# Performance work log

Measured on AMD Instinct MI355X. Metric: run time of the kernel, lower is better.

Reference implementation:

```python
import jax, jax.numpy as jnp
import numpy as np

TEMP = 1.0
NUM_HEADS = 4


def tropical_linear(x, W, b, temperature=TEMP):
    # x: (..., in), W: (out, in), b: (out,)
    # y_i = T * logsumexp_j((W_ij + x_j)/T) + b_i  (soft tropical max-plus)
    z = W + x[..., None, :]                      # (..., out, in) broadcast tensor
    y = temperature * jax.nn.logsumexp(z / temperature, axis=-1)
    return y + b


def setup_inputs() -> dict:
    key = jax.random.key(0)
    ks = jax.random.split(key, 5)
    B, S, E = 32, 64, 256  # seq_len == head_dim (= E / num_heads) required by original code
    x = jax.random.normal(ks[0], (B, S, E), dtype=jnp.float32)
    mk = lambda k: 0.1 * jax.random.normal(k, (E, E), dtype=jnp.float32)
    zb = jnp.zeros((E,), dtype=jnp.float32)
    return {
        "x": x,
        "Wq": mk(ks[1]), "bq": zb,
        "Wk": mk(ks[2]), "bk": zb,
        "Wv": mk(ks[3]), "bv": zb,
        "Wo": mk(ks[4]), "bo": zb,
    }


def reference(x, Wq, bq, Wk, bk, Wv, bv, Wo, bo):
    B, S, E = x.shape
    H = NUM_HEADS
    D = E // H  # == S by construction (required by original matmul)

    q = tropical_linear(x, Wq, bq)  # (B,S,E)
    k = tropical_linear(x, Wk, bk)
    v = tropical_linear(x, Wv, bv)

    # (B,S,E) -> (B,H,S,D)
    split = lambda t: t.reshape(B, S, H, D).transpose(0, 2, 1, 3)
    q, k, v = split(q), split(k), split(v)

    # Original: (q.unsqueeze(-1) + k.unsqueeze(-2).transpose(-1,-2)).sum(-1)
    # Both operands are (B,H,S,D,1) -> scores == q + k elementwise, shape (B,H,S,D).
    scores = q + k
    attn = jax.nn.softmax(scores / TEMP, axis=-1)  # (B,H,S,D)

    # matmul (B,H,S,D) @ (B,H,S,D) valid since D == S
    out = jnp.einsum('bhsd,bhde->bhse', attn, v)   # (B,H,S,D)
    out = out.transpose(0, 2, 1, 3).reshape(B, S, E)
    return tropical_linear(out, Wo, bo)
```

## Files before the change

kernel.cpp:

```cpp
#include <hip/hip_runtime.h>

constexpr int ED = 256;
constexpr int SD = 64;
constexpr int BD = 32;
constexpr int NROWS = BD * SD;
constexpr int RB = 4;

__device__ inline unsigned short f2bf(float f) {
  unsigned u = __float_as_uint(f);
  return (unsigned short)((u + 0x7fffu + ((u >> 16) & 1u)) >> 16);
}
__device__ inline float bf2f(unsigned short b) {
  return __uint_as_float(((unsigned)b) << 16);
}

__global__ __launch_bounds__(256) void expT_pack_kernel(
    const float* __restrict__ Wq, const float* __restrict__ Wk,
    const float* __restrict__ Wv, const float* __restrict__ Wo,
    unsigned int* __restrict__ EqkT, unsigned short* __restrict__ EvT,
    unsigned short* __restrict__ EoT)
{
  __shared__ float ta[32][33], tb[32][33];
  int tx = threadIdx.x & 31, ty = threadIdx.x >> 5;
  int i0 = blockIdx.y * 32, j0 = blockIdx.x * 32;
  const float* A = blockIdx.z ? Wv : Wq;
  const float* Bm = blockIdx.z ? Wo : Wk;
#pragma unroll
  for (int r = 0; r < 4; r++) {
    ta[ty + 8 * r][tx] = __expf(A [(i0 + ty + 8 * r) * ED + j0 + tx]);
    tb[ty + 8 * r][tx] = __expf(Bm[(i0 + ty + 8 * r) * ED + j0 + tx]);
  }
  __syncthreads();
  if (blockIdx.z == 0) {
#pragma unroll
    for (int r = 0; r < 4; r++)
      EqkT[(j0 + ty + 8 * r) * ED + i0 + tx] =
          ((unsigned)f2bf(tb[tx][ty + 8 * r]) << 16) | f2bf(ta[tx][ty + 8 * r]);
  } else {
#pragma unroll
    for (int r = 0; r < 4; r++) {
      EvT[(j0 + ty + 8 * r) * ED + i0 + tx] = f2bf(ta[tx][ty + 8 * r]);
      EoT[(j0 + ty + 8 * r) * ED + i0 + tx] = f2bf(tb[tx][ty + 8 * r]);
    }
  }
}

__global__ __launch_bounds__(1024, 8) void qkv_kernel(
    const float* __restrict__ x,
    const unsigned int* __restrict__ EqkT, const unsigned short* __restrict__ EvT,
    const float* __restrict__ bq, const float* __restrict__ bk,
    const float* __restrict__ bv,
    float* __restrict__ attn, float* __restrict__ vout)
{
  int tid = threadIdx.x;
  int wv = tid >> 6, lane = tid & 63;
  int g = tid >> 8, t = tid & 255;
  int row0 = blockIdx.x * RB;

  __shared__ float eT[ED][RB];
  __shared__ float part[3][RB][ED][4];
  __shared__ float red[RB][4];

  {
    int pr = wv & 3, ps = wv >> 2;
    float xv = x[(size_t)(row0 + pr) * ED + ps * 64 + lane];
    float m = xv;
#pragma unroll
    for (int off = 32; off > 0; off >>= 1) m = fmaxf(m, __shfl_xor(m, off));
    if (lane == 0) red[pr][ps] = m;
    __syncthreads();
    float M = fmaxf(fmaxf(red[pr][0], red[pr][1]), fmaxf(red[pr][2], red[pr][3]));
    eT[ps * 64 + lane][pr] = __expf(xv - M);
  }
  __syncthreads();

  float aq[RB] = {0, 0, 0, 0}, ak[RB] = {0, 0, 0, 0}, av_[RB] = {0, 0, 0, 0};
  const unsigned int*  pqk = EqkT + (size_t)(64 * g) * ED + t;
  const unsigned short* pv = EvT + (size_t)(64 * g) * ED + t;
#pragma unroll 4
  for (int j = 0; j < 64; ++j) {
    float4 e4 = *(const float4*)eT[64 * g + j];
    unsigned int wqk = pqk[j * ED];
    float wvv = bf2f(pv[j * ED]);
    float wq = __uint_as_float(wqk << 16);
    float wk = __uint_as_float(wqk & 0xffff0000u);
    aq[0] = fmaf(wq, e4.x, aq[0]);  ak[0] = fmaf(wk, e4.x, ak[0]);  av_[0] = fmaf(wvv, e4.x, av_[0]);
    aq[1] = fmaf(wq, e4.y, aq[1]);  ak[1] = fmaf(wk, e4.y, ak[1]);  av_[1] = fmaf(wvv, e4.y, av_[1]);
    aq[2] = fmaf(wq, e4.z, aq[2]);  ak[2] = fmaf(wk, e4.z, ak[2]);  av_[2] = fmaf(wvv, e4.z, av_[2]);
    aq[3] = fmaf(wq, e4.w, aq[3]);  ak[3] = fmaf(wk, e4.w, ak[3]);  av_[3] = fmaf(wvv, e4.w, av_[3]);
  }

#pragma unroll
  for (int r = 0; r < RB; r++) {
    part[0][r][t][g] = aq[r];
    part[1][r][t][g] = ak[r];
    part[2][r][t][g] = av_[r];
  }
  __syncthreads();

  float4 q4 = *(const float4*)part[0][g][t];
  float4 k4 = *(const float4*)part[1][g][t];
  float4 v4 = *(const float4*)part[2][g][t];
  float fq = (q4.x + q4.y) + (q4.z + q4.w);
  float fk = (k4.x + k4.y) + (k4.z + k4.w);
  float fv = (v4.x + v4.y) + (v4.z + v4.w);
  float Mr = fmaxf(fmaxf(red[g][0], red[g][1]), fmaxf(red[g][2], red[g][3]));
  float qv = Mr + __logf(fq) + bq[t];
  float kv = Mr + __logf(fk) + bk[t];
  float vv = Mr + __logf(fv) + bv[t];
  vout[(size_t)(row0 + g) * ED + t] = vv;
  float s = qv + kv;
  float sm = s;
#pragma unroll
  for (int off = 32; off > 0; off >>= 1) sm = fmaxf(sm, __shfl_xor(sm, off));
  float ex = __expf(s - sm);
  float den = ex;
#pragma unroll
  for (int off = 32; off > 0; off >>= 1) den += __shfl_xor(den, off);
  attn[(size_t)(row0 + g) * ED + t] = ex / den;
}

__global__ __launch_bounds__(1024, 8) void avo_kernel(
    const float* __restrict__ attn, const float* __restrict__ vbuf,
    const unsigned short* __restrict__ EoT, const float* __restrict__ bo,
    float* __restrict__ y)
{
  int tid = threadIdx.x;
  int wv = tid >> 6, lane = tid & 63;
  int g = tid >> 8, t = tid & 255;
  int b = blockIdx.x >> 4;
  int row0 = b * SD + (blockIdx.x & 15) * RB;

  __shared__ float att[RB][ED];
  __shared__ float part[RB][ED][4];
  __shared__ float eoT[ED][RB];
  __shared__ float red[RB][4];

  att[g][t] = attn[(size_t)(row0 + g) * ED + t];
  float vr[16];
#pragma unroll
  for (int d = 0; d < 16; ++d)
    vr[d] = vbuf[(size_t)(b * SD + 16 * g + d) * ED + t];
  __syncthreads();

  int h64 = (t >> 6) << 6;
  float acc[RB];
#pragma unroll
  for (int r = 0; r < RB; ++r) {
    const float4* ap = (const float4*)&att[r][h64 + 16 * g];
    float a = 0.f;
#pragma unroll
    for (int d4 = 0; d4 < 4; ++d4) {
      float4 a4 = ap[d4];
      a = fmaf(a4.x, vr[4 * d4 + 0], a);
      a = fmaf(a4.y, vr[4 * d4 + 1], a);
      a = fmaf(a4.z, vr[4 * d4 + 2], a);
      a = fmaf(a4.w, vr[4 * d4 + 3], a);
    }
    acc[r] = a;
  }
#pragma unroll
  for (int r = 0; r < RB; ++r) part[r][t][g] = acc[r];
  __syncthreads();

  float4 p4 = *(const float4*)part[g][t];
  float orow = (p4.x + p4.y) + (p4.z + p4.w);
  float m = orow;
#pragma unroll
  for (int off = 32; off > 0; off >>= 1) m = fmaxf(m, __shfl_xor(m, off));
  if (lane == 0) red[g][wv & 3] = m;
  __syncthreads();
  float M = fmaxf(fmaxf(red[g][0], red[g][1]), fmaxf(red[g][2], red[g][3]));
  eoT[t][g] = __expf(orow - M);
  __syncthreads();

  float acc2[RB] = {0, 0, 0, 0};
  const unsigned short* po = EoT + (size_t)(64 * g) * ED + t;
#pragma unroll 4
  for (int j = 0; j < 64; ++j) {
    float4 e4 = *(const float4*)eoT[64 * g + j];
    float wo = bf2f(po[j * ED]);
    acc2[0] = fmaf(wo, e4.x, acc2[0]);
    acc2[1] = fmaf(wo, e4.y, acc2[1]);
    acc2[2] = fmaf(wo, e4.z, acc2[2]);
    acc2[3] = fmaf(wo, e4.w, acc2[3]);
  }
  __syncthreads();
#pragma unroll
  for (int r = 0; r < RB; ++r) part[r][t][g] = acc2[r];
  __syncthreads();

  float4 f4 = *(const float4*)part[g][t];
  float f = (f4.x + f4.y) + (f4.z + f4.w);
  y[(size_t)(row0 + g) * ED + t] = M + __logf(f) + bo[t];
}

extern "C" void kernel_launch(void* const* d_in, const int* in_sizes, int n_in,
                              void* d_out, int out_size, void* d_ws, size_t ws_size,
                              hipStream_t stream) {
  const float* x  = (const float*)d_in[0];
  const float* Wq = (const float*)d_in[1];
  const float* bq = (const float*)d_in[2];
  const float* Wk = (const float*)d_in[3];
  const float* bk = (const float*)d_in[4];
  const float* Wv = (const float*)d_in[5];
  const float* bv = (const float*)d_in[6];
  const float* Wo = (const float*)d_in[7];
  const float* bo = (const float*)d_in[8];
  float* y = (float*)d_out;

  char* ws = (char*)d_ws;
  unsigned int*   EqkT = (unsigned int*)(ws);
  unsigned short* EvT  = (unsigned short*)(ws + 262144);
  unsigned short* EoT  = (unsigned short*)(ws + 393216);
  float* attn = (float*)(ws + 524288);
  float* vbuf = (float*)(ws + 524288 + (size_t)NROWS * ED * 4);

  expT_pack_kernel<<<dim3(8, 8, 2), 256, 0, stream>>>(Wq, Wk, Wv, Wo,
                                                      EqkT, EvT, EoT);
  qkv_kernel<<<NROWS / RB, 1024, 0, stream>>>(x, EqkT, EvT, bq, bk, bv,
                                              attn, vbuf);
  avo_kernel<<<NROWS / RB, 1024, 0, stream>>>(attn, vbuf, EoT, bo, y);
}
```

Measured before the change: 98.72 us.

## Compute QKV tropical projections with bf16 MFMA on swizzled exp-weights

```diff
diff --git a/kernel.cpp b/kernel.cpp
--- a/kernel.cpp
+++ b/kernel.cpp
@@ -6,6 +6,9 @@
 constexpr int NROWS = BD * SD;
 constexpr int RB = 4;
 
+typedef short short8 __attribute__((ext_vector_type(8)));
+typedef float floatx4 __attribute__((ext_vector_type(4)));
+
 __device__ inline unsigned short f2bf(float f) {
   unsigned u = __float_as_uint(f);
   return (unsigned short)((u + 0x7fffu + ((u >> 16) & 1u)) >> 16);
@@ -14,110 +17,130 @@
   return __uint_as_float(((unsigned)b) << 16);
 }
 
-__global__ __launch_bounds__(256) void expT_pack_kernel(
+__global__ __launch_bounds__(256) void expT_swz_kernel(
     const float* __restrict__ Wq, const float* __restrict__ Wk,
-    const float* __restrict__ Wv, const float* __restrict__ Wo,
-    unsigned int* __restrict__ EqkT, unsigned short* __restrict__ EvT,
-    unsigned short* __restrict__ EoT)
-{
-  __shared__ float ta[32][33], tb[32][33];
+    const float* __restrict__ Wv,
+    unsigned short* __restrict__ EqS, unsigned short* __restrict__ EkS,
+    unsigned short* __restrict__ EvS)
+{
+  int z = blockIdx.y;
+  const float* W = (z == 0) ? Wq : (z == 1) ? Wk : Wv;
+  unsigned short* out = (z == 0) ? EqS : (z == 1) ? EkS : EvS;
+  int t = threadIdx.x;
+  int n = blockIdx.x * 8 + (t >> 5), kl = t & 31;
+#pragma unroll
+  for (int kk = 0; kk < 8; ++kk) {
+    float v = __expf(W[n * ED + 32 * kk + kl]);
+    out[(kk * 256 + n) * 32 + kl] = f2bf(v);
+  }
+}
+
+__global__ __launch_bounds__(256) void expT_o_kernel(
+    const float* __restrict__ Wo, unsigned short* __restrict__ EoT)
+{
+  __shared__ float ta[32][33];
   int tx = threadIdx.x & 31, ty = threadIdx.x >> 5;
   int i0 = blockIdx.y * 32, j0 = blockIdx.x * 32;
-  const float* A = blockIdx.z ? Wv : Wq;
-  const float* Bm = blockIdx.z ? Wo : Wk;
-#pragma unroll
-  for (int r = 0; r < 4; r++) {
-    ta[ty + 8 * r][tx] = __expf(A [(i0 + ty + 8 * r) * ED + j0 + tx]);
-    tb[ty + 8 * r][tx] = __expf(Bm[(i0 + ty + 8 * r) * ED + j0 + tx]);
-  }
-  __syncthreads();
-  if (blockIdx.z == 0) {
-#pragma unroll
-    for (int r = 0; r < 4; r++)
-      EqkT[(j0 + ty + 8 * r) * ED + i0 + tx] =
-          ((unsigned)f2bf(tb[tx][ty + 8 * r]) << 16) | f2bf(ta[tx][ty + 8 * r]);
-  } else {
-#pragma unroll
-    for (int r = 0; r < 4; r++) {
-      EvT[(j0 + ty + 8 * r) * ED + i0 + tx] = f2bf(ta[tx][ty + 8 * r]);
-      EoT[(j0 + ty + 8 * r) * ED + i0 + tx] = f2bf(tb[tx][ty + 8 * r]);
-    }
-  }
-}
-
-__global__ __launch_bounds__(1024, 8) void qkv_kernel(
+#pragma unroll
+  for (int r = 0; r < 4; r++)
+    ta[ty + 8 * r][tx] = __expf(Wo[(i0 + ty + 8 * r) * ED + j0 + tx]);
+  __syncthreads();
+#pragma unroll
+  for (int r = 0; r < 4; r++)
+    EoT[(j0 + ty + 8 * r) * ED + i0 + tx] = f2bf(ta[tx][ty + 8 * r]);
+}
+
+__global__ __launch_bounds__(256, 4) void qkv_mfma_kernel(
     const float* __restrict__ x,
-    const unsigned int* __restrict__ EqkT, const unsigned short* __restrict__ EvT,
+    const unsigned short* __restrict__ EqS, const unsigned short* __restrict__ EkS,
+    const unsigned short* __restrict__ EvS,
     const float* __restrict__ bq, const float* __restrict__ bk,
     const float* __restrict__ bv,
     float* __restrict__ attn, float* __restrict__ vout)
 {
-  int tid = threadIdx.x;
-  int wv = tid >> 6, lane = tid & 63;
-  int g = tid >> 8, t = tid & 255;
-  int row0 = blockIdx.x * RB;
-
-  __shared__ float eT[ED][RB];
-  __shared__ float part[3][RB][ED][4];
-  __shared__ float red[RB][4];
+  int t = threadIdx.x;
+  int w = t >> 6, lane = t & 63;
+  int mt = blockIdx.x >> 2, h = blockIdx.x & 3;
+  int row0 = mt * 16;
+
+  __shared__ unsigned short aswz[8 * 512];
+  __shared__ float fbuf[3][16][65];
+  __shared__ float Mrow[16];
+
+#pragma unroll
+  for (int i = 0; i < 4; ++i) {
+    int r = 4 * w + i;
+    float4 xv = *(const float4*)&x[(size_t)(row0 + r) * ED + lane * 4];
+    float m = fmaxf(fmaxf(xv.x, xv.y), fmaxf(xv.z, xv.w));
+#pragma unroll
+    for (int off = 32; off > 0; off >>= 1) m = fmaxf(m, __shfl_xor(m, off));
+    ushort4 pk;
+    pk.x = f2bf(__expf(xv.x - m));
+    pk.y = f2bf(__expf(xv.y - m));
+    pk.z = f2bf(__expf(xv.z - m));
+    pk.w = f2bf(__expf(xv.w - m));
+    int k0 = lane * 4;
+    int idx = (k0 >> 5) * 512 + ((k0 >> 3) & 3) * 128 + r * 8 + (k0 & 7);
+    *(ushort4*)&aswz[idx] = pk;
+    if (lane == 0) Mrow[r] = m;
+  }
+  __syncthreads();
+
+  short8 afrag[8];
+#pragma unroll
+  for (int kk = 0; kk < 8; ++kk)
+    afrag[kk] = *(const short8*)&aswz[kk * 512 + lane * 8];
+
+  int bb = ((h * 64 + w * 16 + (lane & 15)) << 2) + (w >> 2, lane >> 4);
+  bb = ((h * 64 + w * 16 + (lane & 15)) << 2) + (lane >> 4);
+  const short8* BQ = (const short8*)EqS;
+  const short8* BK = (const short8*)EkS;
+  const short8* BV = (const short8*)EvS;
+  floatx4 accq = {0.f, 0.f, 0.f, 0.f};
+  floatx4 acck = {0.f, 0.f, 0.f, 0.f};
+  floatx4 accv = {0.f, 0.f, 0.f, 0.f};
+#pragma unroll
+  for (int kk = 0; kk < 8; ++kk) {
+    short8 bqf = BQ[kk * 1024 + bb];
+    short8 bkf = BK[kk * 1024 + bb];
+    short8 bvf = BV[kk * 1024 + bb];
+    accq = __builtin_amdgcn_mfma_f32_16x16x32_bf16(afrag[kk], bqf, accq, 0, 0, 0);
+    acck = __builtin_amdgcn_mfma_f32_16x16x32_bf16(afrag[kk], bkf, acck, 0, 0, 0);
+    accv = __builtin_amdgcn_mfma_f32_16x16x32_bf16(afrag[kk], bvf, accv, 0, 0, 0);
+  }
 
   {
-    int pr = wv & 3, ps = wv >> 2;
-    float xv = x[(size_t)(row0 + pr) * ED + ps * 64 + lane];
-    float m = xv;
-#pragma unroll
-    for (int off = 32; off > 0; off >>= 1) m = fmaxf(m, __shfl_xor(m, off));
-    if (lane == 0) red[pr][ps] = m;
-    __syncthreads();
-    float M = fmaxf(fmaxf(red[pr][0], red[pr][1]), fmaxf(red[pr][2], red[pr][3]));
-    eT[ps * 64 + lane][pr] = __expf(xv - M);
-  }
-  __syncthreads();
-
-  float aq[RB] = {0, 0, 0, 0}, ak[RB] = {0, 0, 0, 0}, av_[RB] = {0, 0, 0, 0};
-  const unsigned int*  pqk = EqkT + (size_t)(64 * g) * ED + t;
-  const unsigned short* pv = EvT + (size_t)(64 * g) * ED + t;
-#pragma unroll 4
-  for (int j = 0; j < 64; ++j) {
-    float4 e4 = *(const float4*)eT[64 * g + j];
-    unsigned int wqk = pqk[j * ED];
-    float wvv = bf2f(pv[j * ED]);
-    float wq = __uint_as_float(wqk << 16);
-    float wk = __uint_as_float(wqk & 0xffff0000u);
-    aq[0] = fmaf(wq, e4.x, aq[0]);  ak[0] = fmaf(wk, e4.x, ak[0]);  av_[0] = fmaf(wvv, e4.x, av_[0]);
-    aq[1] = fmaf(wq, e4.y, aq[1]);  ak[1] = fmaf(wk, e4.y, ak[1]);  av_[1] = fmaf(wvv, e4.y, av_[1]);
-    aq[2] = fmaf(wq, e4.z, aq[2]);  ak[2] = fmaf(wk, e4.z, ak[2]);  av_[2] = fmaf(wvv, e4.z, av_[2]);
-    aq[3] = fmaf(wq, e4.w, aq[3]);  ak[3] = fmaf(wk, e4.w, ak[3]);  av_[3] = fmaf(wvv, e4.w, av_[3]);
-  }
-
-#pragma unroll
-  for (int r = 0; r < RB; r++) {
-    part[0][r][t][g] = aq[r];
-    part[1][r][t][g] = ak[r];
-    part[2][r][t][g] = av_[r];
-  }
-  __syncthreads();
-
-  float4 q4 = *(const float4*)part[0][g][t];
-  float4 k4 = *(const float4*)part[1][g][t];
-  float4 v4 = *(const float4*)part[2][g][t];
-  float fq = (q4.x + q4.y) + (q4.z + q4.w);
-  float fk = (k4.x + k4.y) + (k4.z + k4.w);
-  float fv = (v4.x + v4.y) + (v4.z + v4.w);
-  float Mr = fmaxf(fmaxf(red[g][0], red[g][1]), fmaxf(red[g][2], red[g][3]));
-  float qv = Mr + __logf(fq) + bq[t];
-  float kv = Mr + __logf(fk) + bk[t];
-  float vv = Mr + __logf(fv) + bv[t];
-  vout[(size_t)(row0 + g) * ED + t] = vv;
-  float s = qv + kv;
-  float sm = s;
-#pragma unroll
-  for (int off = 32; off > 0; off >>= 1) sm = fmaxf(sm, __shfl_xor(sm, off));
-  float ex = __expf(s - sm);
-  float den = ex;
-#pragma unroll
-  for (int off = 32; off > 0; off >>= 1) den += __shfl_xor(den, off);
-  attn[(size_t)(row0 + g) * ED + t] = ex / den;
+    int c = w * 16 + (lane & 15);
+    int rb = (lane >> 4) * 4;
+#pragma unroll
+    for (int reg = 0; reg < 4; ++reg) {
+      fbuf[0][rb + reg][c] = accq[reg];
+      fbuf[1][rb + reg][c] = acck[reg];
+      fbuf[2][rb + reg][c] = accv[reg];
+    }
+  }
+  __syncthreads();
+
+  int cg = h * 64 + lane;
+  float bqv = bq[cg], bkv = bk[cg], bvv = bv[cg];
+#pragma unroll
+  for (int i = 0; i < 4; ++i) {
+    int r = 4 * w + i;
+    float Mr = Mrow[r];
+    float qv = Mr + __logf(fbuf[0][r][lane]) + bqv;
+    float kv = Mr + __logf(fbuf[1][r][lane]) + bkv;
+    float vv = Mr + __logf(fbuf[2][r][lane]) + bvv;
+    vout[(size_t)(row0 + r) * ED + cg] = vv;
+    float s = qv + kv;
+    float sm = s;
+#pragma unroll
+    for (int off = 32; off > 0; off >>= 1) sm = fmaxf(sm, __shfl_xor(sm, off));
+    float ex = __expf(s - sm);
+    float den = ex;
+#pragma unroll
+    for (int off = 32; off > 0; off >>= 1) den += __shfl_xor(den, off);
+    attn[(size_t)(row0 + r) * ED + cg] = ex / den;
+  }
 }
 
 __global__ __launch_bounds__(1024, 8) void avo_kernel(
@@ -210,15 +233,16 @@
   float* y = (float*)d_out;
 
   char* ws = (char*)d_ws;
-  unsigned int*   EqkT = (unsigned int*)(ws);
-  unsigned short* EvT  = (unsigned short*)(ws + 262144);
-  unsigned short* EoT  = (unsigned short*)(ws + 393216);
+  unsigned short* EqS = (unsigned short*)(ws);
+  unsigned short* EkS = (unsigned short*)(ws + 131072);
+  unsigned short* EvS = (unsigned short*)(ws + 262144);
+  unsigned short* EoT = (unsigned short*)(ws + 393216);
   float* attn = (float*)(ws + 524288);
   float* vbuf = (float*)(ws + 524288 + (size_t)NROWS * ED * 4);
 
-  expT_pack_kernel<<<dim3(8, 8, 2), 256, 0, stream>>>(Wq, Wk, Wv, Wo,
-                                                      EqkT, EvT, EoT);
-  qkv_kernel<<<NROWS / RB, 1024, 0, stream>>>(x, EqkT, EvT, bq, bk, bv,
-                                              attn, vbuf);
+  expT_swz_kernel<<<dim3(32, 3), 256, 0, stream>>>(Wq, Wk, Wv, EqS, EkS, EvS);
+  expT_o_kernel<<<dim3(8, 8), 256, 0, stream>>>(Wo, EoT);
+  qkv_mfma_kernel<<<512, 256, 0, stream>>>(x, EqS, EkS, EvS, bq, bk, bv,
+                                           attn, vbuf);
   avo_kernel<<<NROWS / RB, 1024, 0, stream>>>(attn, vbuf, EoT, bo, y);
 }
```

New measurement: 96.04 us. 1.03x faster.
